# Performance work log

Hardware: AMD Instinct MI355X
Metric: run time of the kernel (lower is better)

## Reference

```python
import jax, jax.numpy as jnp
import numpy as np

N, E, IN_CH, EDGE_DIM, N_GRAPHS = 8000, 64000, 256, 16, 64
HEADS = (3, 2, 2, 1)
OUT_CH = (512, 512, 256, 256)
IN_CHS = (IN_CH, 1536, 1024, 512)
NEG_SLOPE = 0.2  # PyG GATv2Conv default negative_slope


def setup_inputs() -> dict:
    key = jax.random.key(0)
    ks = iter(jax.random.split(key, 64))
    d = {}
    d["x"] = jax.random.normal(next(ks), (N, IN_CH), jnp.float32)
    d["edge_index"] = jax.random.randint(next(ks), (2, E), 0, N, dtype=jnp.int32)
    d["edge_attr"] = jax.random.normal(next(ks), (E, EDGE_DIM), jnp.float32)
    d["batch"] = jnp.sort(jax.random.randint(next(ks), (N,), 0, N_GRAPHS, dtype=jnp.int32))
    for i, (ci, h, co) in enumerate(zip(IN_CHS, HEADS, OUT_CH), 1):
        hc = h * co
        s = 1.0 / np.sqrt(ci)
        d[f"W{i}l"] = (jax.random.normal(next(ks), (ci, hc)) * s).astype(jnp.float32)
        d[f"b{i}l"] = jnp.zeros((hc,), jnp.float32)
        d[f"W{i}r"] = (jax.random.normal(next(ks), (ci, hc)) * s).astype(jnp.float32)
        d[f"b{i}r"] = jnp.zeros((hc,), jnp.float32)
        d[f"W{i}e"] = (jax.random.normal(next(ks), (EDGE_DIM, hc)) / np.sqrt(EDGE_DIM)).astype(jnp.float32)
        d[f"att{i}"] = (jax.random.normal(next(ks), (h, co)) / np.sqrt(co)).astype(jnp.float32)
        d[f"bias{i}"] = jnp.zeros((hc,), jnp.float32)
    d["fc1_w"] = (jax.random.normal(next(ks), (256, 64)) / 16.0).astype(jnp.float32)
    d["fc1_b"] = jnp.zeros((64,), jnp.float32)
    d["fc2_w"] = (jax.random.normal(next(ks), (64, 1)) / 8.0).astype(jnp.float32)
    d["fc2_b"] = jnp.zeros((1,), jnp.float32)
    return d


def gatv2(x, src, dst, ea, Wl, bl, Wr, br, We, att, bias, heads, co):
    """GATv2Conv forward (PyG semantics, self-loops already appended in src/dst/ea)."""
    n = x.shape[0]
    xl = (x @ Wl + bl).reshape(n, heads, co)  # applied to source nodes
    xr = (x @ Wr + br).reshape(n, heads, co)  # applied to target nodes
    ee = (ea @ We).reshape(-1, heads, co)     # edge embedding (no bias in PyG)
    m = xl[src] + xr[dst] + ee                # [E', H, C]
    logits = jnp.einsum('ehc,hc->eh', jax.nn.leaky_relu(m, NEG_SLOPE), att)
    # segmented softmax over incoming edges per destination node
    lmax = jax.ops.segment_max(logits, dst, num_segments=n)
    p = jnp.exp(logits - lmax[dst])
    denom = jax.ops.segment_sum(p, dst, num_segments=n)
    alpha = p / denom[dst]                    # every node has a self-loop -> denom > 0
    out = jax.ops.segment_sum(alpha[:, :, None] * xl[src], dst, num_segments=n)
    return out.reshape(n, heads * co) + bias


def _forward(x, edge_index, edge_attr, batch, params, fc):
    n = x.shape[0]
    src0, dst0 = edge_index[0], edge_index[1]
    # add_self_loops with fill_value='mean': per-destination mean of incoming edge_attr
    ea_sum = jax.ops.segment_sum(edge_attr, dst0, num_segments=n)
    ea_cnt = jax.ops.segment_sum(jnp.ones((edge_attr.shape[0], 1), edge_attr.dtype), dst0, num_segments=n)
    ea_loop = ea_sum / jnp.maximum(ea_cnt, 1.0)
    loop = jnp.arange(n, dtype=edge_index.dtype)
    src = jnp.concatenate([src0, loop])
    dst = jnp.concatenate([dst0, loop])
    ea = jnp.concatenate([edge_attr, ea_loop])
    h = x
    for p, hds, co in zip(params, HEADS, OUT_CH):
        h = jax.nn.relu(gatv2(h, src, dst, ea, *p, hds, co))
    # global mean pool over graphs
    s = jax.ops.segment_sum(h, batch, num_segments=N_GRAPHS)
    cnt = jax.ops.segment_sum(jnp.ones((n, 1), h.dtype), batch, num_segments=N_GRAPHS)
    g = s / jnp.maximum(cnt, 1.0)
    # dropout is identity in eval mode
    fc1_w, fc1_b, fc2_w, fc2_b = fc
    g = jax.nn.relu(g @ fc1_w + fc1_b)
    return g @ fc2_w + fc2_b


def reference(x, edge_index, edge_attr, batch,
              W1l, b1l, W1r, b1r, W1e, att1, bias1,
              W2l, b2l, W2r, b2r, W2e, att2, bias2,
              W3l, b3l, W3r, b3r, W3e, att3, bias3,
              W4l, b4l, W4r, b4r, W4e, att4, bias4,
              fc1_w, fc1_b, fc2_w, fc2_b):
    params = [(W1l, b1l, W1r, b1r, W1e, att1, bias1),
              (W2l, b2l, W2r, b2r, W2e, att2, bias2),
              (W3l, b3l, W3r, b3r, W3e, att3, bias3),
              (W4l, b4l, W4r, b4r, W4e, att4, bias4)]
    return _forward(x, edge_index, edge_attr, batch, params, (fc1_w, fc1_b, fc2_w, fc2_b))
```

## Files before the change

### kernel.cpp

```cpp
#include <hip/hip_runtime.h>
#include <math.h>

#define N_NODES 8000
#define N_EDGES 64000
#define ETOT    (N_EDGES + N_NODES)
#define EDIM    16
#define NGRAPHS 64

typedef __attribute__((ext_vector_type(8))) short short8v;
typedef __attribute__((ext_vector_type(4))) short short4v;
typedef __attribute__((ext_vector_type(4))) float f32x4;

__device__ inline unsigned short f2bf(float f) {
    unsigned u = __builtin_bit_cast(unsigned, f);
    unsigned r = (u + 0x7FFF + ((u >> 16) & 1)) >> 16;
    return (unsigned short)r;
}
__device__ inline float bf2f(unsigned short b) {
    unsigned u = ((unsigned)b) << 16;
    return __builtin_bit_cast(float, u);
}


__global__ void count_deg(const int* __restrict__ dst0, int* __restrict__ deg) {
    int e = blockIdx.x * 256 + threadIdx.x;
    if (e < N_EDGES) atomicAdd(&deg[dst0[e]], 1);
}

__global__ void scan_deg(const int* __restrict__ deg, int* __restrict__ rowptr) {
    __shared__ int sh[256];
    __shared__ int carry_s;
    int t = threadIdx.x;
    if (t == 0) { carry_s = 0; rowptr[0] = 0; }
    __syncthreads();
    for (int base = 0; base < N_NODES; base += 256) {
        int i = base + t;
        int v = (i < N_NODES) ? (deg[i] + 1) : 0;
        sh[t] = v;
        __syncthreads();
        for (int off = 1; off < 256; off <<= 1) {
            int u = (t >= off) ? sh[t - off] : 0;
            __syncthreads();
            sh[t] += u;
            __syncthreads();
        }
        int incl = sh[t] + carry_s;
        if (i < N_NODES) rowptr[i + 1] = incl;
        __syncthreads();
        if (t == 255) carry_s = incl;
        __syncthreads();
    }
}

__global__ void copy_off(const int* __restrict__ rowptr, int* __restrict__ woff) {
    int i = blockIdx.x * 256 + threadIdx.x;
    if (i < N_NODES) woff[i] = rowptr[i];
}

__global__ void fill_eid(const int* __restrict__ dst0, int* __restrict__ woff,
                         int* __restrict__ eid) {
    int i = blockIdx.x * 256 + threadIdx.x;
    if (i < N_EDGES) {
        int pos = atomicAdd(&woff[dst0[i]], 1);
        eid[pos] = i;
    } else if (i < ETOT) {
        int n = i - N_EDGES;
        int pos = atomicAdd(&woff[n], 1);
        eid[pos] = i;
    }
}

__global__ void csr_fill_dst(const int* __restrict__ rowptr, int* __restrict__ csr_dst) {
    int n = blockIdx.x * 256 + threadIdx.x;
    if (n >= N_NODES) return;
    int b = rowptr[n], t = rowptr[n + 1];
    for (int i = b; i < t; i++) csr_dst[i] = n;
}

__global__ void ea_loop_kernel(const int* __restrict__ rowptr, const int* __restrict__ eid,
                               const float* __restrict__ edge_attr, float* __restrict__ ea_loop) {
    int n = blockIdx.x * 256 + threadIdx.x;
    if (n >= N_NODES) return;
    float s[EDIM];
#pragma unroll
    for (int k = 0; k < EDIM; k++) s[k] = 0.f;
    int cnt = 0;
    int b = rowptr[n], t = rowptr[n + 1];
    for (int i = b; i < t; i++) {
        int e = eid[i];
        if (e < N_EDGES) {
            cnt++;
            const float* ea = edge_attr + (size_t)e * EDIM;
#pragma unroll
            for (int k = 0; k < EDIM; k++) s[k] += ea[k];
        }
    }
    float inv = 1.f / (float)(cnt > 0 ? cnt : 1);
#pragma unroll
    for (int k = 0; k < EDIM; k++) ea_loop[(size_t)n * EDIM + k] = s[k] * inv;
}

__global__ void csr_srcea(const int* __restrict__ eid, const int* __restrict__ src0,
                          const float* __restrict__ edge_attr, const float* __restrict__ ea_loop,
                          int* __restrict__ csr_src, float* __restrict__ ea_csr) {
    int t = blockIdx.x * 256 + threadIdx.x;
    int i = t >> 2, q = t & 3;
    if (i >= ETOT) return;
    int e = eid[i];
    int s = (e < N_EDGES) ? src0[e] : (e - N_EDGES);
    if (q == 0) csr_src[i] = s;
    const float* ea = (e < N_EDGES) ? edge_attr + (size_t)e * EDIM
                                    : ea_loop + (size_t)(e - N_EDGES) * EDIM;
    *(float4*)(ea_csr + (size_t)i * EDIM + q * 4) = *(const float4*)(ea + q * 4);
}

__global__ void cvt_ea(const float* __restrict__ ea_csr,
                       short* __restrict__ eah, short* __restrict__ eal) {
    int t = blockIdx.x * 256 + threadIdx.x;
    if (t >= ETOT * EDIM) return;
    int e = t >> 4, k = t & 15;
    float v = ea_csr[(size_t)e * EDIM + k];
    unsigned short h = f2bf(v);
    unsigned short l = f2bf(v - bf2f(h));
    eah[(size_t)e * 32 + k] = (short)h;
    eal[(size_t)e * 32 + k] = (short)l;
    eah[(size_t)e * 32 + 16 + k] = 0;
    eal[(size_t)e * 32 + 16 + k] = 0;
}

__global__ void cvt_we(const float* __restrict__ We,
                       short* __restrict__ weTh, short* __restrict__ weTl, int hc) {
    int ch = blockIdx.x * 256 + threadIdx.x;
    if (ch >= hc) return;
#pragma unroll
    for (int k = 0; k < EDIM; k++) {
        float v = We[(size_t)k * hc + ch];
        unsigned short h = f2bf(v);
        unsigned short l = f2bf(v - bf2f(h));
        weTh[(size_t)ch * 32 + k] = (short)h;
        weTl[(size_t)ch * 32 + k] = (short)l;
    }
#pragma unroll
    for (int k = EDIM; k < 32; k++) {
        weTh[(size_t)ch * 32 + k] = 0;
        weTl[(size_t)ch * 32 + k] = 0;
    }
}


__global__ __launch_bounds__(256) void cvt_wt_t(
        const float* __restrict__ W, short* __restrict__ WTh, short* __restrict__ WTl,
        int K, int Nc) {
    __shared__ float sh[32][33];
    int t = threadIdx.x;
    int tx = t & 31, ty = t >> 5;
    int n0 = blockIdx.x * 32, k0 = blockIdx.y * 32;
#pragma unroll
    for (int j = 0; j < 4; j++)
        sh[ty + j * 8][tx] = W[(size_t)(k0 + ty + j * 8) * Nc + n0 + tx];
    __syncthreads();
#pragma unroll
    for (int j = 0; j < 4; j++) {
        int row = ty + j * 8;
        float v = sh[tx][row];
        unsigned short h = f2bf(v);
        unsigned short l = f2bf(v - bf2f(h));
        size_t idx = (size_t)(n0 + row) * K + k0 + tx;
        WTh[idx] = (short)h;
        WTl[idx] = (short)l;
    }
}


__global__ __launch_bounds__(256) void cvt_act(
        const float* __restrict__ in, short* __restrict__ acth, short* __restrict__ actl,
        int total ) {
    int i = blockIdx.x * 256 + threadIdx.x;
    if (i * 4 >= total) return;
    float4 v = *(const float4*)(in + (size_t)i * 4);
    unsigned short h0 = f2bf(v.x), h1 = f2bf(v.y), h2 = f2bf(v.z), h3 = f2bf(v.w);
    short4v hv = { (short)h0, (short)h1, (short)h2, (short)h3 };
    short4v lv = { (short)f2bf(v.x - bf2f(h0)), (short)f2bf(v.y - bf2f(h1)),
                   (short)f2bf(v.z - bf2f(h2)), (short)f2bf(v.w - bf2f(h3)) };
    *(short4v*)(acth + (size_t)i * 4) = hv;
    *(short4v*)(actl + (size_t)i * 4) = lv;
}


#define LDK 40

__global__ __launch_bounds__(256) void gemm_mfma2(
        const short* __restrict__ Ah_g, const short* __restrict__ Al_g,
        const short* __restrict__ BTh, const short* __restrict__ BTl,
        const float* __restrict__ bias, float* __restrict__ C,
        int M, int K, int Nc) {
    __shared__ short Ah[128 * LDK];
    __shared__ short Al[128 * LDK];
    __shared__ short Bh[128 * LDK];
    __shared__ short Bl[128 * LDK];
    int t = threadIdx.x;
    int m0 = blockIdx.y * 128, n0 = blockIdx.x * 128;
    int lane = t & 63, wave = t >> 6;
    int wm = (wave >> 1) * 64, wn = (wave & 1) * 64;
    int fr = lane & 15, koff = (lane >> 4) * 8;

    f32x4 acc[4][4];
#pragma unroll
    for (int i = 0; i < 4; i++)
#pragma unroll
        for (int j = 0; j < 4; j++) acc[i][j] = (f32x4)(0.f);

    int srow = t >> 1, sseg = t & 1;

    for (int k0 = 0; k0 < K; k0 += 32) {
        __syncthreads();
        {
            const short* ga_h = Ah_g + (size_t)(m0 + srow) * K + k0 + sseg * 16;
            const short* ga_l = Al_g + (size_t)(m0 + srow) * K + k0 + sseg * 16;
            const short* gb_h = BTh + (size_t)(n0 + srow) * K + k0 + sseg * 16;
            const short* gb_l = BTl + (size_t)(n0 + srow) * K + k0 + sseg * 16;
            int lo = srow * LDK + sseg * 16;
            *(short8v*)&Ah[lo]     = *(const short8v*)ga_h;
            *(short8v*)&Ah[lo + 8] = *(const short8v*)(ga_h + 8);
            *(short8v*)&Al[lo]     = *(const short8v*)ga_l;
            *(short8v*)&Al[lo + 8] = *(const short8v*)(ga_l + 8);
            *(short8v*)&Bh[lo]     = *(const short8v*)gb_h;
            *(short8v*)&Bh[lo + 8] = *(const short8v*)(gb_h + 8);
            *(short8v*)&Bl[lo]     = *(const short8v*)gb_l;
            *(short8v*)&Bl[lo + 8] = *(const short8v*)(gb_l + 8);
        }
        __syncthreads();

        short8v ah[4], al[4], bh[4], bl[4];
#pragma unroll
        for (int mi = 0; mi < 4; mi++) {
            int r = (wm + mi * 16 + fr) * LDK + koff;
            ah[mi] = *(short8v*)&Ah[r];
            al[mi] = *(short8v*)&Al[r];
        }
#pragma unroll
        for (int ni = 0; ni < 4; ni++) {
            int r = (wn + ni * 16 + fr) * LDK + koff;
            bh[ni] = *(short8v*)&Bh[r];
            bl[ni] = *(short8v*)&Bl[r];
        }
#pragma unroll
        for (int mi = 0; mi < 4; mi++)
#pragma unroll
            for (int ni = 0; ni < 4; ni++) {
                acc[mi][ni] = __builtin_amdgcn_mfma_f32_16x16x32_bf16(
                    al[mi], bh[ni], acc[mi][ni], 0, 0, 0);
                acc[mi][ni] = __builtin_amdgcn_mfma_f32_16x16x32_bf16(
                    ah[mi], bl[ni], acc[mi][ni], 0, 0, 0);
                acc[mi][ni] = __builtin_amdgcn_mfma_f32_16x16x32_bf16(
                    ah[mi], bh[ni], acc[mi][ni], 0, 0, 0);
            }
    }

    int rbase = (lane >> 4) * 4;
#pragma unroll
    for (int ni = 0; ni < 4; ni++) {
        int col = n0 + wn + ni * 16 + fr;
        float bz = bias[col];
#pragma unroll
        for (int mi = 0; mi < 4; mi++) {
            int row0 = m0 + wm + mi * 16 + rbase;
#pragma unroll
            for (int r = 0; r < 4; r++) {
                int row = row0 + r;
                if (row < M) C[(size_t)row * Nc + col] = acc[mi][ni][r] + bz;
            }
        }
    }
}


__global__ __launch_bounds__(256) void gemm_mfma(
        const float* __restrict__ A, const short* __restrict__ BTh,
        const short* __restrict__ BTl, const float* __restrict__ bias,
        float* __restrict__ C, int M, int K, int Nc) {
    __shared__ short Ah[128 * LDK];
    __shared__ short Al[128 * LDK];
    __shared__ short Bh[128 * LDK];
    __shared__ short Bl[128 * LDK];
    int t = threadIdx.x;
    int m0 = blockIdx.y * 128, n0 = blockIdx.x * 128;
    int lane = t & 63, wave = t >> 6;
    int wm = (wave >> 1) * 64, wn = (wave & 1) * 64;
    int fr = lane & 15, koff = (lane >> 4) * 8;

    f32x4 acc[4][4];
#pragma unroll
    for (int i = 0; i < 4; i++)
#pragma unroll
        for (int j = 0; j < 4; j++) acc[i][j] = (f32x4)(0.f);

    int brow = t >> 1, bseg = t & 1;

    for (int k0 = 0; k0 < K; k0 += 32) {
        __syncthreads();
#pragma unroll
        for (int i = 0; i < 4; i++) {
            int f = t + i * 256;
            int row = f >> 3, seg = f & 7;
            float4 v = make_float4(0.f, 0.f, 0.f, 0.f);
            if (m0 + row < M)
                v = *(const float4*)(A + (size_t)(m0 + row) * K + k0 + seg * 4);
            unsigned short h0 = f2bf(v.x), h1 = f2bf(v.y), h2 = f2bf(v.z), h3 = f2bf(v.w);
            short4v hv = { (short)h0, (short)h1, (short)h2, (short)h3 };
            short4v lv = { (short)f2bf(v.x - bf2f(h0)), (short)f2bf(v.y - bf2f(h1)),
                           (short)f2bf(v.z - bf2f(h2)), (short)f2bf(v.w - bf2f(h3)) };
            *(short4v*)&Ah[row * LDK + seg * 4] = hv;
            *(short4v*)&Al[row * LDK + seg * 4] = lv;
        }
        {
            const short* gh = BTh + (size_t)(n0 + brow) * K + k0 + bseg * 16;
            const short* gl = BTl + (size_t)(n0 + brow) * K + k0 + bseg * 16;
            int lo = brow * LDK + bseg * 16;
            *(short8v*)&Bh[lo]     = *(const short8v*)gh;
            *(short8v*)&Bh[lo + 8] = *(const short8v*)(gh + 8);
            *(short8v*)&Bl[lo]     = *(const short8v*)gl;
            *(short8v*)&Bl[lo + 8] = *(const short8v*)(gl + 8);
        }
        __syncthreads();

        short8v ah[4], al[4], bh[4], bl[4];
#pragma unroll
        for (int mi = 0; mi < 4; mi++) {
            int r = (wm + mi * 16 + fr) * LDK + koff;
            ah[mi] = *(short8v*)&Ah[r];
            al[mi] = *(short8v*)&Al[r];
        }
#pragma unroll
        for (int ni = 0; ni < 4; ni++) {
            int r = (wn + ni * 16 + fr) * LDK + koff;
            bh[ni] = *(short8v*)&Bh[r];
            bl[ni] = *(short8v*)&Bl[r];
        }
#pragma unroll
        for (int mi = 0; mi < 4; mi++)
#pragma unroll
            for (int ni = 0; ni < 4; ni++) {
                acc[mi][ni] = __builtin_amdgcn_mfma_f32_16x16x32_bf16(
                    al[mi], bh[ni], acc[mi][ni], 0, 0, 0);
                acc[mi][ni] = __builtin_amdgcn_mfma_f32_16x16x32_bf16(
                    ah[mi], bl[ni], acc[mi][ni], 0, 0, 0);
                acc[mi][ni] = __builtin_amdgcn_mfma_f32_16x16x32_bf16(
                    ah[mi], bh[ni], acc[mi][ni], 0, 0, 0);
            }
    }

    int rbase = (lane >> 4) * 4;
#pragma unroll
    for (int ni = 0; ni < 4; ni++) {
        int col = n0 + wn + ni * 16 + fr;
        float bz = bias[col];
#pragma unroll
        for (int mi = 0; mi < 4; mi++) {
            int row0 = m0 + wm + mi * 16 + rbase;
#pragma unroll
            for (int r = 0; r < 4; r++) {
                int row = row0 + r;
                if (row < M) C[(size_t)row * Nc + col] = acc[mi][ni][r] + bz;
            }
        }
    }
}


__global__ __launch_bounds__(256) void edge_logits6(
        const float* __restrict__ xl, const float* __restrict__ xr,
        const short* __restrict__ weTh, const short* __restrict__ weTl,
        const float* __restrict__ att,
        const short* __restrict__ eah, const short* __restrict__ eal,
        const int* __restrict__ csr_src, const int* __restrict__ csr_dst,
        float* __restrict__ logits, int H, int co_shift, int hc) {
    int tid = threadIdx.x;
    int lane = tid & 63, wave = tid >> 6;
    int cbase = blockIdx.y << 8;
    int head = cbase >> co_shift;
    int e0 = blockIdx.x * 64 + wave * 16;
    int col = lane & 15;
    int quad = lane >> 4;
    int e = e0 + col;
    int s = csr_src[e], d = csr_dst[e];
    int ch0 = cbase + quad * 4;

    short8v bh = *(const short8v*)(eah + (size_t)e * 32 + quad * 8);
    short8v bl = *(const short8v*)(eal + (size_t)e * 32 + quad * 8);

    const float* xls = xl + (size_t)s * hc + ch0;
    const float* xrd = xr + (size_t)d * hc + ch0;
    const float* atp = att + ch0;
    const short* wph = weTh + (size_t)(cbase + col) * 32 + quad * 8;
    const short* wpl = weTl + (size_t)(cbase + col) * 32 + quad * 8;

    float p = 0.f;
#pragma unroll
    for (int tt = 0; tt < 16; tt++) {
        short8v ah = *(const short8v*)(wph + (size_t)tt * 16 * 32);
        short8v al = *(const short8v*)(wpl + (size_t)tt * 16 * 32);
        f32x4 ee = (f32x4)(0.f);
        ee = __builtin_amdgcn_mfma_f32_16x16x32_bf16(ah, bl, ee, 0, 0, 0);
        ee = __builtin_amdgcn_mfma_f32_16x16x32_bf16(al, bh, ee, 0, 0, 0);
        ee = __builtin_amdgcn_mfma_f32_16x16x32_bf16(ah, bh, ee, 0, 0, 0);
        float4 lv = *(const float4*)(xls + tt * 16);
        float4 rv = *(const float4*)(xrd + tt * 16);
        float4 av = *(const float4*)(atp + tt * 16);
        float m0 = lv.x + rv.x + ee[0];
        float m1 = lv.y + rv.y + ee[1];
        float m2 = lv.z + rv.z + ee[2];
        float m3 = lv.w + rv.w + ee[3];
        m0 = (m0 > 0.f) ? m0 : 0.2f * m0;
        m1 = (m1 > 0.f) ? m1 : 0.2f * m1;
        m2 = (m2 > 0.f) ? m2 : 0.2f * m2;
        m3 = (m3 > 0.f) ? m3 : 0.2f * m3;
        p += m0 * av.x + m1 * av.y + m2 * av.z + m3 * av.w;
    }
    p += __shfl_down(p, 32, 64);
    p += __shfl_down(p, 16, 64);
    if (lane < 16)
        atomicAdd(&logits[(size_t)(e0 + lane) * H + head], p);
}


__global__ __launch_bounds__(256) void aggregate4(
        const int* __restrict__ rowptr, const int* __restrict__ csr_src,
        const float* __restrict__ logits, const float* __restrict__ xl,
        const float* __restrict__ bias, float* __restrict__ out,
        int H, int co_shift, int hc) {
    __shared__ int ssrc[64];
    __shared__ float salp[64][4];
    __shared__ float sm[4], sinv[4];
    int n = blockIdx.x;
    int b = rowptr[n], t = rowptr[n + 1];
    int tid = threadIdx.x;
    int nthr = blockDim.x;

    if (tid < H) {
        float m = -1e30f;
        for (int i = b; i < t; i++)
            m = fmaxf(m, logits[(size_t)i * H + tid]);
        float s = 0.f;
        for (int i = b; i < t; i++)
            s += expf(logits[(size_t)i * H + tid] - m);
        sm[tid] = m;
        sinv[tid] = 1.f / s;
    }
    __syncthreads();

    int j0 = tid * 4;
    int j1 = j0 + nthr * 4;
    int h0 = j0 >> co_shift;
    int h1 = j1 >> co_shift;
    bool act1 = j1 < hc;

    float4 acc0 = make_float4(0.f, 0.f, 0.f, 0.f);
    float4 acc1 = make_float4(0.f, 0.f, 0.f, 0.f);

    for (int cb = b; cb < t; cb += 64) {
        int m = min(64, t - cb);
        __syncthreads();
        for (int i = tid; i < m; i += nthr) {
            ssrc[i] = csr_src[cb + i];
            for (int h = 0; h < H; h++)
                salp[i][h] = expf(logits[(size_t)(cb + i) * H + h] - sm[h]) * sinv[h];
        }
        __syncthreads();
        for (int i = 0; i < m; i++) {
            int s = ssrc[i];
            const float* base = xl + (size_t)s * hc;
            {
                float a = salp[i][h0];
                float4 v = *(const float4*)(base + j0);
                acc0.x += a * v.x; acc0.y += a * v.y;
                acc0.z += a * v.z; acc0.w += a * v.w;
            }
            if (act1) {
                float a = salp[i][h1];
                float4 v = *(const float4*)(base + j1);
                acc1.x += a * v.x; acc1.y += a * v.y;
                acc1.z += a * v.z; acc1.w += a * v.w;
            }
        }
    }
    {
        float4 bz = *(const float4*)(bias + j0);
        float4 o;
        o.x = fmaxf(acc0.x + bz.x, 0.f); o.y = fmaxf(acc0.y + bz.y, 0.f);
        o.z = fmaxf(acc0.z + bz.z, 0.f); o.w = fmaxf(acc0.w + bz.w, 0.f);
        *(float4*)(out + (size_t)n * hc + j0) = o;
    }
    if (act1) {
        float4 bz = *(const float4*)(bias + j1);
        float4 o;
        o.x = fmaxf(acc1.x + bz.x, 0.f); o.y = fmaxf(acc1.y + bz.y, 0.f);
        o.z = fmaxf(acc1.z + bz.z, 0.f); o.w = fmaxf(acc1.w + bz.w, 0.f);
        *(float4*)(out + (size_t)n * hc + j1) = o;
    }
}


__global__ void pool_cnt(const int* __restrict__ batch, int* __restrict__ gcnt) {
    int n = blockIdx.x * 256 + threadIdx.x;
    if (n < N_NODES) atomicAdd(&gcnt[batch[n]], 1);
}

__global__ void pool_sum(const int* __restrict__ batch, const float* __restrict__ h,
                         float* __restrict__ pooled) {
    int tid = blockIdx.x * 256 + threadIdx.x;
    if (tid >= N_NODES * 256) return;
    int n = tid >> 8, c = tid & 255;
    atomicAdd(&pooled[batch[n] * 256 + c], h[tid]);
}

__global__ void mlp_head(const float* __restrict__ pooled, const int* __restrict__ gcnt,
                         const float* __restrict__ fc1w, const float* __restrict__ fc1b,
                         const float* __restrict__ fc2w, const float* __restrict__ fc2b,
                         float* __restrict__ out) {
    int g = threadIdx.x;
    if (g >= NGRAPHS) return;
    float inv = 1.f / (float)(gcnt[g] > 0 ? gcnt[g] : 1);
    float s[64];
#pragma unroll
    for (int j = 0; j < 64; j++) s[j] = fc1b[j];
    for (int c = 0; c < 256; c++) {
        float mv = pooled[g * 256 + c] * inv;
#pragma unroll
        for (int j = 0; j < 64; j++) s[j] += mv * fc1w[c * 64 + j];
    }
    float o = 0.f;
#pragma unroll
    for (int j = 0; j < 64; j++) o += fmaxf(s[j], 0.f) * fc2w[j];
    out[g] = o + fc2b[0];
}


extern "C" void kernel_launch(void* const* d_in, const int* in_sizes, int n_in,
                              void* d_out, int out_size, void* d_ws, size_t ws_size,
                              hipStream_t stream) {
    const float* x         = (const float*)d_in[0];
    const int*   edge_index= (const int*)d_in[1];
    const float* edge_attr = (const float*)d_in[2];
    const int*   batch     = (const int*)d_in[3];
    const int* src0 = edge_index;
    const int* dst0 = edge_index + N_EDGES;

    const float *Wl[4], *bl[4], *Wr[4], *br[4], *We[4], *att[4], *bias[4];
    for (int i = 0; i < 4; i++) {
        int base = 4 + 7 * i;
        Wl[i]   = (const float*)d_in[base + 0];
        bl[i]   = (const float*)d_in[base + 1];
        Wr[i]   = (const float*)d_in[base + 2];
        br[i]   = (const float*)d_in[base + 3];
        We[i]   = (const float*)d_in[base + 4];
        att[i]  = (const float*)d_in[base + 5];
        bias[i] = (const float*)d_in[base + 6];
    }
    const float* fc1w = (const float*)d_in[32];
    const float* fc1b = (const float*)d_in[33];
    const float* fc2w = (const float*)d_in[34];
    const float* fc2b = (const float*)d_in[35];
    float* out = (float*)d_out;

    float* ws = (float*)d_ws;
    int*   rowptr  = (int*)(ws + 0);
    int*   woff    = (int*)(ws + 8064);
    int*   eid     = (int*)(ws + 16128);
    int*   csr_src = (int*)(ws + 88128);
    int*   csr_dst = (int*)(ws + 160128);
    float* ea_loop = ws + 232128;
    float* ea_csr  = ws + 360128;
    float* logits  = ws + 1512128;
    float* xl      = ws + 1728128;
    float* xr      = xl  + 12288000;
    float* hbF     = xr  + 12288000;
    float* pooled  = hbF + 12288000;
    int*   gcnt    = (int*)(pooled + 16384);
    short* wth     = (short*)(ws + 38608640);
    short* wtl     = (short*)(ws + 39788288);
    short* eah     = (short*)(ws + 40967936);
    short* eal     = (short*)(ws + 42119936);
    short* weTh    = (short*)(ws + 43271936);
    short* weTl    = (short*)(ws + 43296512);
    short* acth    = (short*)(ws + 43321088);
    short* actl    = (short*)(ws + 49514240);
    const size_t NEED_PRESPLIT = (size_t)55707392 * 4;
    bool presplit = ws_size >= NEED_PRESPLIT;

    hipMemsetAsync(woff, 0, N_NODES * sizeof(int), stream);
    count_deg<<<(N_EDGES + 255) / 256, 256, 0, stream>>>(dst0, woff);
    scan_deg<<<1, 256, 0, stream>>>(woff, rowptr);
    copy_off<<<(N_NODES + 255) / 256, 256, 0, stream>>>(rowptr, woff);
    fill_eid<<<(ETOT + 255) / 256, 256, 0, stream>>>(dst0, woff, eid);
    csr_fill_dst<<<(N_NODES + 255) / 256, 256, 0, stream>>>(rowptr, csr_dst);
    ea_loop_kernel<<<(N_NODES + 255) / 256, 256, 0, stream>>>(rowptr, eid, edge_attr, ea_loop);
    csr_srcea<<<(ETOT * 4 + 255) / 256, 256, 0, stream>>>(eid, src0, edge_attr, ea_loop,
                                                          csr_src, ea_csr);
    cvt_ea<<<(ETOT * EDIM + 255) / 256, 256, 0, stream>>>(ea_csr, eah, eal);

    const int IN[4] = {256, 1536, 1024, 512};
    const int HH[4] = {3, 2, 2, 1};
    const int CO[4] = {512, 512, 256, 256};
    const int CS[4] = {9, 9, 8, 8};
    const float* hin = x;

    for (int L = 0; L < 4; L++) {
        int K = IN[L], H = HH[L], co = CO[L], hc = H * co, cs = CS[L];
        (void)co;
        dim3 gg(hc / 128, (N_NODES + 127) / 128);
        dim3 gw(hc / 32, K / 32);
        if (presplit) {
            int total = N_NODES * K;
            cvt_act<<<(total / 4 + 255) / 256, 256, 0, stream>>>(hin, acth, actl, total);
            cvt_wt_t<<<gw, 256, 0, stream>>>(Wl[L], wth, wtl, K, hc);
            gemm_mfma2<<<gg, 256, 0, stream>>>(acth, actl, wth, wtl, bl[L], xl, N_NODES, K, hc);
            cvt_wt_t<<<gw, 256, 0, stream>>>(Wr[L], wth, wtl, K, hc);
            gemm_mfma2<<<gg, 256, 0, stream>>>(acth, actl, wth, wtl, br[L], xr, N_NODES, K, hc);
        } else {
            cvt_wt_t<<<gw, 256, 0, stream>>>(Wl[L], wth, wtl, K, hc);
            gemm_mfma<<<gg, 256, 0, stream>>>(hin, wth, wtl, bl[L], xl, N_NODES, K, hc);
            cvt_wt_t<<<gw, 256, 0, stream>>>(Wr[L], wth, wtl, K, hc);
            gemm_mfma<<<gg, 256, 0, stream>>>(hin, wth, wtl, br[L], xr, N_NODES, K, hc);
        }
        cvt_we<<<(hc + 255) / 256, 256, 0, stream>>>(We[L], weTh, weTl, hc);
        hipMemsetAsync(logits, 0, (size_t)ETOT * H * sizeof(float), stream);
        dim3 gl(ETOT / 64, hc / 256);
        edge_logits6<<<gl, 256, 0, stream>>>(
            xl, xr, weTh, weTl, att[L], eah, eal, csr_src, csr_dst, logits, H, cs, hc);
        int athr = hc / 4 > 256 ? 256 : hc / 4;
        aggregate4<<<N_NODES, athr, 0, stream>>>(
            rowptr, csr_src, logits, xl, bias[L], hbF, H, cs, hc);
        hin = hbF;
    }

    hipMemsetAsync(pooled, 0, (16384 + 64) * sizeof(float), stream);
    pool_cnt<<<(N_NODES + 255) / 256, 256, 0, stream>>>(batch, gcnt);
    pool_sum<<<(N_NODES * 256 + 255) / 256, 256, 0, stream>>>(batch, hbF, pooled);
    mlp_head<<<1, 64, 0, stream>>>(pooled, gcnt, fc1w, fc1b, fc2w, fc2b, out);
}
```

Before: 1.368 ms.

## Fuse left/right projection GEMMs and compute full-head edge logits without atomics

The Wl and Wr projections are now computed by one GEMM over concatenated transposed weights, writing an interleaved [N, 2*hc] buffer with a per-column choice of bias. The edge logits kernel now gives each block a whole head, so the logit is written directly instead of via atomicAdd after a memset. Its loop software-prefetches the next tile's operands and sets an occupancy hint in launch_bounds. The aims are fewer launches, reuse of the activation tile across both projections, and no memset or atomic traffic. The cost is a strided layout for xl and xr and longer serial loops per block when co is 512.

```diff
diff --git a/kernel.cpp b/kernel.cpp
--- a/kernel.cpp
+++ b/kernel.cpp
@@ -192,8 +192,8 @@
 __global__ __launch_bounds__(256) void gemm_mfma2(
         const short* __restrict__ Ah_g, const short* __restrict__ Al_g,
         const short* __restrict__ BTh, const short* __restrict__ BTl,
-        const float* __restrict__ bias, float* __restrict__ C,
-        int M, int K, int Nc) {
+        const float* __restrict__ bias1, const float* __restrict__ bias2, int hsplit,
+        float* __restrict__ C, int M, int K, int Nc) {
     __shared__ short Ah[128 * LDK];
     __shared__ short Al[128 * LDK];
     __shared__ short Bh[128 * LDK];
@@ -261,7 +261,8 @@
 #pragma unroll
     for (int ni = 0; ni < 4; ni++) {
         int col = n0 + wn + ni * 16 + fr;
-        float bz = bias[col];
+        const float* bp = (col < hsplit) ? bias1 + col : bias2 + (col - hsplit);
+        float bz = *bp;
 #pragma unroll
         for (int mi = 0; mi < 4; mi++) {
             int row0 = m0 + wm + mi * 16 + rbase;
@@ -277,7 +278,8 @@
 
 __global__ __launch_bounds__(256) void gemm_mfma(
         const float* __restrict__ A, const short* __restrict__ BTh,
-        const short* __restrict__ BTl, const float* __restrict__ bias,
+        const short* __restrict__ BTl,
+        const float* __restrict__ bias1, const float* __restrict__ bias2, int hsplit,
         float* __restrict__ C, int M, int K, int Nc) {
     __shared__ short Ah[128 * LDK];
     __shared__ short Al[128 * LDK];
@@ -354,7 +356,8 @@
 #pragma unroll
     for (int ni = 0; ni < 4; ni++) {
         int col = n0 + wn + ni * 16 + fr;
-        float bz = bias[col];
+        const float* bp = (col < hsplit) ? bias1 + col : bias2 + (col - hsplit);
+        float bz = *bp;
 #pragma unroll
         for (int mi = 0; mi < 4; mi++) {
             int row0 = m0 + wm + mi * 16 + rbase;
@@ -368,17 +371,17 @@
 }
 
 
-__global__ __launch_bounds__(256) void edge_logits6(
+__global__ __launch_bounds__(256, 4) void edge_logits7(
         const float* __restrict__ xl, const float* __restrict__ xr,
         const short* __restrict__ weTh, const short* __restrict__ weTl,
         const float* __restrict__ att,
         const short* __restrict__ eah, const short* __restrict__ eal,
         const int* __restrict__ csr_src, const int* __restrict__ csr_dst,
-        float* __restrict__ logits, int H, int co_shift, int hc) {
+        float* __restrict__ logits, int H, int co, int stride) {
     int tid = threadIdx.x;
     int lane = tid & 63, wave = tid >> 6;
-    int cbase = blockIdx.y << 8;
-    int head = cbase >> co_shift;
+    int head = blockIdx.y;
+    int cbase = head * co;
     int e0 = blockIdx.x * 64 + wave * 16;
     int col = lane & 15;
     int quad = lane >> 4;
@@ -389,38 +392,64 @@
     short8v bh = *(const short8v*)(eah + (size_t)e * 32 + quad * 8);
     short8v bl = *(const short8v*)(eal + (size_t)e * 32 + quad * 8);
 
-    const float* xls = xl + (size_t)s * hc + ch0;
-    const float* xrd = xr + (size_t)d * hc + ch0;
+    const float* xls = xl + (size_t)s * stride + ch0;
+    const float* xrd = xr + (size_t)d * stride + ch0;
     const float* atp = att + ch0;
     const short* wph = weTh + (size_t)(cbase + col) * 32 + quad * 8;
     const short* wpl = weTl + (size_t)(cbase + col) * 32 + quad * 8;
 
+    int ntile = co >> 4;
     float p = 0.f;
-#pragma unroll
-    for (int tt = 0; tt < 16; tt++) {
-        short8v ah = *(const short8v*)(wph + (size_t)tt * 16 * 32);
-        short8v al = *(const short8v*)(wpl + (size_t)tt * 16 * 32);
+
+    short8v ahA = *(const short8v*)wph;
+    short8v alA = *(const short8v*)wpl;
+    float4 lvA = *(const float4*)xls;
+    float4 rvA = *(const float4*)xrd;
+    float4 avA = *(const float4*)atp;
+
+    for (int tt = 0; tt < ntile - 1; tt++) {
+        short8v ahB = *(const short8v*)(wph + (size_t)(tt + 1) * 512);
+        short8v alB = *(const short8v*)(wpl + (size_t)(tt + 1) * 512);
+        float4 lvB = *(const float4*)(xls + (tt + 1) * 16);
+        float4 rvB = *(const float4*)(xrd + (tt + 1) * 16);
+        float4 avB = *(const float4*)(atp + (tt + 1) * 16);
+
         f32x4 ee = (f32x4)(0.f);
-        ee = __builtin_amdgcn_mfma_f32_16x16x32_bf16(ah, bl, ee, 0, 0, 0);
-        ee = __builtin_amdgcn_mfma_f32_16x16x32_bf16(al, bh, ee, 0, 0, 0);
-        ee = __builtin_amdgcn_mfma_f32_16x16x32_bf16(ah, bh, ee, 0, 0, 0);
-        float4 lv = *(const float4*)(xls + tt * 16);
-        float4 rv = *(const float4*)(xrd + tt * 16);
-        float4 av = *(const float4*)(atp + tt * 16);
-        float m0 = lv.x + rv.x + ee[0];
-        float m1 = lv.y + rv.y + ee[1];
-        float m2 = lv.z + rv.z + ee[2];
-        float m3 = lv.w + rv.w + ee[3];
+        ee = __builtin_amdgcn_mfma_f32_16x16x32_bf16(ahA, bl, ee, 0, 0, 0);
+        ee = __builtin_amdgcn_mfma_f32_16x16x32_bf16(alA, bh, ee, 0, 0, 0);
+        ee = __builtin_amdgcn_mfma_f32_16x16x32_bf16(ahA, bh, ee, 0, 0, 0);
+        float m0 = lvA.x + rvA.x + ee[0];
+        float m1 = lvA.y + rvA.y + ee[1];
+        float m2 = lvA.z + rvA.z + ee[2];
+        float m3 = lvA.w + rvA.w + ee[3];
         m0 = (m0 > 0.f) ? m0 : 0.2f * m0;
         m1 = (m1 > 0.f) ? m1 : 0.2f * m1;
         m2 = (m2 > 0.f) ? m2 : 0.2f * m2;
         m3 = (m3 > 0.f) ? m3 : 0.2f * m3;
-        p += m0 * av.x + m1 * av.y + m2 * av.z + m3 * av.w;
-    }
+        p += m0 * avA.x + m1 * avA.y + m2 * avA.z + m3 * avA.w;
+
+        ahA = ahB; alA = alB; lvA = lvB; rvA = rvB; avA = avB;
+    }
+    {
+        f32x4 ee = (f32x4)(0.f);
+        ee = __builtin_amdgcn_mfma_f32_16x16x32_bf16(ahA, bl, ee, 0, 0, 0);
+        ee = __builtin_amdgcn_mfma_f32_16x16x32_bf16(alA, bh, ee, 0, 0, 0);
+        ee = __builtin_amdgcn_mfma_f32_16x16x32_bf16(ahA, bh, ee, 0, 0, 0);
+        float m0 = lvA.x + rvA.x + ee[0];
+        float m1 = lvA.y + rvA.y + ee[1];
+        float m2 = lvA.z + rvA.z + ee[2];
+        float m3 = lvA.w + rvA.w + ee[3];
+        m0 = (m0 > 0.f) ? m0 : 0.2f * m0;
+        m1 = (m1 > 0.f) ? m1 : 0.2f * m1;
+        m2 = (m2 > 0.f) ? m2 : 0.2f * m2;
+        m3 = (m3 > 0.f) ? m3 : 0.2f * m3;
+        p += m0 * avA.x + m1 * avA.y + m2 * avA.z + m3 * avA.w;
+    }
+
     p += __shfl_down(p, 32, 64);
     p += __shfl_down(p, 16, 64);
     if (lane < 16)
-        atomicAdd(&logits[(size_t)(e0 + lane) * H + head], p);
+        logits[(size_t)(e0 + lane) * H + head] = p;
 }
 
 
@@ -428,7 +457,7 @@
         const int* __restrict__ rowptr, const int* __restrict__ csr_src,
         const float* __restrict__ logits, const float* __restrict__ xl,
         const float* __restrict__ bias, float* __restrict__ out,
-        int H, int co_shift, int hc) {
+        int H, int co_shift, int hc, int stride) {
     __shared__ int ssrc[64];
     __shared__ float salp[64][4];
     __shared__ float sm[4], sinv[4];
@@ -469,7 +498,7 @@
         __syncthreads();
         for (int i = 0; i < m; i++) {
             int s = ssrc[i];
-            const float* base = xl + (size_t)s * hc;
+            const float* base = xl + (size_t)s * stride;
             {
                 float a = salp[i][h0];
                 float4 v = *(const float4*)(base + j0);
@@ -572,20 +601,19 @@
     float* ea_loop = ws + 232128;
     float* ea_csr  = ws + 360128;
     float* logits  = ws + 1512128;
-    float* xl      = ws + 1728128;
-    float* xr      = xl  + 12288000;
-    float* hbF     = xr  + 12288000;
+    float* xlr     = ws + 1728128;
+    float* hbF     = xlr + 24576000;
     float* pooled  = hbF + 12288000;
     int*   gcnt    = (int*)(pooled + 16384);
     short* wth     = (short*)(ws + 38608640);
-    short* wtl     = (short*)(ws + 39788288);
-    short* eah     = (short*)(ws + 40967936);
-    short* eal     = (short*)(ws + 42119936);
-    short* weTh    = (short*)(ws + 43271936);
-    short* weTl    = (short*)(ws + 43296512);
-    short* acth    = (short*)(ws + 43321088);
-    short* actl    = (short*)(ws + 49514240);
-    const size_t NEED_PRESPLIT = (size_t)55707392 * 4;
+    short* wtl     = (short*)(ws + 40181504);
+    short* eah     = (short*)(ws + 41754368);
+    short* eal     = (short*)(ws + 42906368);
+    short* weTh    = (short*)(ws + 44058368);
+    short* weTl    = (short*)(ws + 44082944);
+    short* acth    = (short*)(ws + 44107520);
+    short* actl    = (short*)(ws + 50300672);
+    const size_t NEED_PRESPLIT = (size_t)56493824 * 4;
     bool presplit = ws_size >= NEED_PRESPLIT;
 
     hipMemsetAsync(woff, 0, N_NODES * sizeof(int), stream);
@@ -607,30 +635,32 @@
 
     for (int L = 0; L < 4; L++) {
         int K = IN[L], H = HH[L], co = CO[L], hc = H * co, cs = CS[L];
-        (void)co;
-        dim3 gg(hc / 128, (N_NODES + 127) / 128);
+        int hc2 = 2 * hc;
+        dim3 gg(hc2 / 128, (N_NODES + 127) / 128);
         dim3 gw(hc / 32, K / 32);
         if (presplit) {
             int total = N_NODES * K;
             cvt_act<<<(total / 4 + 255) / 256, 256, 0, stream>>>(hin, acth, actl, total);
             cvt_wt_t<<<gw, 256, 0, stream>>>(Wl[L], wth, wtl, K, hc);
-            gemm_mfma2<<<gg, 256, 0, stream>>>(acth, actl, wth, wtl, bl[L], xl, N_NODES, K, hc);
-            cvt_wt_t<<<gw, 256, 0, stream>>>(Wr[L], wth, wtl, K, hc);
-            gemm_mfma2<<<gg, 256, 0, stream>>>(acth, actl, wth, wtl, br[L], xr, N_NODES, K, hc);
+            cvt_wt_t<<<gw, 256, 0, stream>>>(Wr[L], wth + (size_t)hc * K,
+                                             wtl + (size_t)hc * K, K, hc);
+            gemm_mfma2<<<gg, 256, 0, stream>>>(acth, actl, wth, wtl,
+                                               bl[L], br[L], hc, xlr, N_NODES, K, hc2);
         } else {
             cvt_wt_t<<<gw, 256, 0, stream>>>(Wl[L], wth, wtl, K, hc);
-            gemm_mfma<<<gg, 256, 0, stream>>>(hin, wth, wtl, bl[L], xl, N_NODES, K, hc);
-            cvt_wt_t<<<gw, 256, 0, stream>>>(Wr[L], wth, wtl, K, hc);
-            gemm_mfma<<<gg, 256, 0, stream>>>(hin, wth, wtl, br[L], xr, N_NODES, K, hc);
+            cvt_wt_t<<<gw, 256, 0, stream>>>(Wr[L], wth + (size_t)hc * K,
+                                             wtl + (size_t)hc * K, K, hc);
+            gemm_mfma<<<gg, 256, 0, stream>>>(hin, wth, wtl,
+                                              bl[L], br[L], hc, xlr, N_NODES, K, hc2);
         }
         cvt_we<<<(hc + 255) / 256, 256, 0, stream>>>(We[L], weTh, weTl, hc);
-        hipMemsetAsync(logits, 0, (size_t)ETOT * H * sizeof(float), stream);
-        dim3 gl(ETOT / 64, hc / 256);
-        edge_logits6<<<gl, 256, 0, stream>>>(
-            xl, xr, weTh, weTl, att[L], eah, eal, csr_src, csr_dst, logits, H, cs, hc);
+        dim3 gl(ETOT / 64, H);
+        edge_logits7<<<gl, 256, 0, stream>>>(
+            xlr, xlr + hc, weTh, weTl, att[L], eah, eal, csr_src, csr_dst,
+            logits, H, co, hc2);
         int athr = hc / 4 > 256 ? 256 : hc / 4;
         aggregate4<<<N_NODES, athr, 0, stream>>>(
-            rowptr, csr_src, logits, xl, bias[L], hbF, H, cs, hc);
+            rowptr, csr_src, logits, xlr, bias[L], hbF, H, cs, hc, hc2);
         hin = hbF;
     }
 
```

New measurement: 1.270 ms. -7.1%, faster.
